# Performance work log

Hardware: AMD Instinct MI355X
Metric: run time of the kernel (lower is better)

Reference implementation:

```python
import jax, jax.numpy as jnp
import numpy as np

D_MODEL = 1024
N_HEAD = 16
HEAD_DIM = D_MODEL // N_HEAD  # 64


def setup_inputs() -> dict:
    key = jax.random.key(0)
    ks = jax.random.split(key, 8)
    B, T, C = 4, 2048, D_MODEL
    s = 0.02
    return {
        "q": jax.random.normal(ks[0], (B, T, C), jnp.float32),
        "k": jax.random.normal(ks[1], (B, T, C), jnp.float32),
        "v": jax.random.normal(ks[2], (B, T, C), jnp.float32),
        "Wq": jax.random.normal(ks[3], (C, C), jnp.float32) * s,
        "Wk": jax.random.normal(ks[4], (C, HEAD_DIM), jnp.float32) * s,
        "Wv": jax.random.normal(ks[5], (C, HEAD_DIM), jnp.float32) * s,
        "Wp": jax.random.normal(ks[6], (C, C), jnp.float32) * s,
        "bp": jnp.zeros((C,), jnp.float32),
    }


def reference(q, k, v, Wq, Wk, Wv, Wp, bp):
    B, T, C = q.shape
    scale = 1.0 / jnp.sqrt(jnp.asarray(HEAD_DIM, q.dtype))
    # projections (torch Linear: x @ W.T, here weights stored as [in, out])
    q_proj = (q @ Wq).reshape(B, T, N_HEAD, HEAD_DIM)  # [B,T,H,D]
    k_proj = k @ Wk  # [B,T,D] single shared KV head
    v_proj = v @ Wv  # [B,T,D]
    # full O(T^2) scores per head, shared K
    wei = jnp.einsum("bqhd,bkd->bhqk", q_proj, k_proj) * scale  # [B,H,T,T]
    p = jax.nn.softmax(wei, axis=-1)
    out = jnp.einsum("bhqk,bkd->bqhd", p, v_proj).reshape(B, T, C)
    return out @ Wp + bp  # dropout p=0.0 -> identity
```

## Files before the change

kernel.cpp:

```cpp
#include <hip/hip_runtime.h>
#include <hip/hip_bf16.h>


#define B_ 4
#define T_ 2048
#define C_ 1024
#define H_ 16
#define D_ 64
#define BT_ (B_*T_)
#define CS_ 0.1803368801111204f

typedef short bfrag __attribute__((ext_vector_type(8)));
typedef float f32x4 __attribute__((ext_vector_type(4)));
typedef __bf16 bf2_t __attribute__((ext_vector_type(2)));

static __device__ inline short f2bf(float f){
    union { __bf16 h; short s; } c; c.h = (__bf16)f;
    return c.s;
}
static __device__ inline unsigned pk2(float a, float b){
    union { bf2_t v; unsigned u; } c;
    c.v[0] = (__bf16)a; c.v[1] = (__bf16)b;
    return c.u;
}

#if __has_builtin(__builtin_amdgcn_global_load_lds)
#define GLL16(g,l) __builtin_amdgcn_global_load_lds(                              \
    (const __attribute__((address_space(1))) void*)(g),                           \
    (__attribute__((address_space(3))) void*)(l), 16, 0, 0)
#else
#define GLL16(g,l) (*(uint4*)(l) = *(const uint4*)(g))
#endif

#if __has_builtin(__builtin_amdgcn_exp2f)
#define EXP2(x) __builtin_amdgcn_exp2f(x)
#else
#define EXP2(x) __expf((x)*0.693147180559945f)
#endif

__global__ __launch_bounds__(256) void prep_kernel(
    const float* __restrict__ Wq, const float* __restrict__ Wk,
    const float* __restrict__ Wv, const float* __restrict__ Wp,
    short* __restrict__ WqT, short* __restrict__ WkT,
    short* __restrict__ WvT, short* __restrict__ WpT)
{
    int b2 = blockIdx.x, tid = threadIdx.x;
    __shared__ short Ls[64][65];
    const float* W; short* Wt; int N, idx;
    if (b2 < 256)      { W = Wq; Wt = WqT; N = 1024; idx = b2; }
    else if (b2 < 272) { W = Wk; Wt = WkT; N = 64;   idx = b2 - 256; }
    else if (b2 < 288) { W = Wv; Wt = WvT; N = 64;   idx = b2 - 272; }
    else               { W = Wp; Wt = WpT; N = 1024; idx = b2 - 288; }
    int nx = N >> 6;
    int n0 = (idx % nx) * 64, k0 = (idx / nx) * 64;
    {
        int kr = tid >> 2, c4 = (tid & 3) * 16;
        const float* g = W + (size_t)(k0 + kr) * N + n0 + c4;
        #pragma unroll
        for (int e = 0; e < 16; e++) Ls[kr][c4 + e] = f2bf(g[e]);
    }
    __syncthreads();
    {
        int nr = tid >> 2, kc = (tid & 3) * 16;
        __align__(16) short tmp[16];
        #pragma unroll
        for (int e = 0; e < 16; e++) tmp[e] = Ls[kc + e][nr];
        short* o = Wt + (size_t)(n0 + nr) * 1024 + k0 + kc;
        *(uint4*)(o)     = *(uint4*)tmp;
        *(uint4*)(o + 8) = *(uint4*)(tmp + 8);
    }
}

__global__ __launch_bounds__(256) void proj_kernel(
    const float* __restrict__ Aq, const float* __restrict__ Ksrc,
    const float* __restrict__ Vsrc,
    const short* __restrict__ WqT, const short* __restrict__ WkT,
    const short* __restrict__ WvT,
    short* __restrict__ Qp, short* __restrict__ Kfo, short* __restrict__ Vfo)
{
    __shared__ __align__(16) short lds[16384];
    int bx = blockIdx.x, tid = threadIdx.x;
    int w = tid >> 6, lane = tid & 63;
    int quad = lane >> 4, l16 = lane & 15;

    if (bx < 512) {
        short* As = lds;
        short* Bs = lds + 8192;
        const int K = C_;
        int wm = (w >> 1) * 64, wn = (w & 1) * 64;
        int m0 = (bx & 63) * 128, n0 = (bx >> 6) * 128;

        const float* gA[8]; short* lA[8];
        #pragma unroll
        for (int i = 0; i < 8; i++) {
            int c = tid + 256 * i;
            int row = c >> 4, fc = c & 15;
            gA[i] = Aq + (size_t)(m0 + row) * K + fc * 4;
            int m16 = row >> 4, l16r = row & 15;
            int ks = fc >> 3, q4 = (fc >> 1) & 3, e0 = (fc & 1) * 4;
            lA[i] = As + ((m16 * 2 + ks) * 64 + l16r * 4 + q4) * 8 + e0;
        }
        const short* gB[4]; short* lB[4];
        #pragma unroll
        for (int i = 0; i < 4; i++) {
            int c = tid + 256 * i;
            int row = ((c >> 7) << 4) + ((c & 63) >> 2);
            int koff = ((c >> 6) & 1) * 32 + (c & 3) * 8;
            gB[i] = WqT + (size_t)(n0 + row) * K + koff;
            lB[i] = Bs + c * 8;
        }

        f32x4 acc[4][4] = {};
        for (int k0 = 0; k0 < K; k0 += 64) {
            __syncthreads();
            #pragma unroll
            for (int i = 0; i < 8; i++) {
                float4 f = *(const float4*)(gA[i] + k0);
                uint2 p; p.x = pk2(f.x, f.y); p.y = pk2(f.z, f.w);
                *(uint2*)lA[i] = p;
            }
            #pragma unroll
            for (int i = 0; i < 4; i++) GLL16(gB[i] + k0, lB[i]);
            __syncthreads();
            #pragma unroll
            for (int ks = 0; ks < 2; ks++) {
                bfrag af[4], bf[4];
                #pragma unroll
                for (int i = 0; i < 4; i++)
                    af[i] = *(const bfrag*)(As + ((((wm >> 4) + i) * 2 + ks) * 64 + l16 * 4 + quad) * 8);
                #pragma unroll
                for (int i = 0; i < 4; i++)
                    bf[i] = *(const bfrag*)(Bs + ((((wn >> 4) + i) * 2 + ks) * 64 + l16 * 4 + quad) * 8);
                #pragma unroll
                for (int mi = 0; mi < 4; mi++)
                    #pragma unroll
                    for (int ni = 0; ni < 4; ni++)
                        acc[mi][ni] = __builtin_amdgcn_mfma_f32_16x16x32_bf16(af[mi], bf[ni], acc[mi][ni], 0, 0, 0);
            }
        }
        #pragma unroll
        for (int mi = 0; mi < 4; mi++)
            #pragma unroll
            for (int ni = 0; ni < 4; ni++) {
                int col = n0 + wn + ni * 16 + l16;
                #pragma unroll
                for (int r = 0; r < 4; r++) {
                    int row = m0 + wm + mi * 16 + quad * 4 + r;
                    Qp[(size_t)row * C_ + col] = f2bf(acc[mi][ni][r] * CS_);
                }
            }
        return;
    }

    {
        short* As = lds;
        short* Bs = lds + 2048;
        int idx2 = bx - 512;
        int mode = idx2 >> 8;
        int m0 = (idx2 & 255) * 32;
        const float* A  = mode ? Vsrc : Ksrc;
        const short* Bt = mode ? WvT : WkT;
        short* Out      = mode ? Vfo : Kfo;

        int wrow = (w >> 1) * 16, wcol = (w & 1) * 32;

        int arow = tid >> 3, acol = (tid & 7) * 8;
        int akh = acol >> 5, aoct = (acol >> 3) & 3;
        short* asl = As + ((((arow >> 4) * 2 + akh) * 64 + (arow & 15) * 4 + aoct) * 8);
        const float* ag = A + (size_t)(m0 + arow) * C_ + acol;
        int brow = tid >> 2, bcol = (tid & 3) * 16;
        int bkh = bcol >> 5, boct = (bcol >> 3) & 3;
        short* bsl = Bs + ((((brow >> 4) * 2 + bkh) * 64 + (brow & 15) * 4 + boct) * 8);
        const short* bg = Bt + (size_t)brow * C_ + bcol;

        f32x4 acc[2] = {};
        for (int k0 = 0; k0 < C_; k0 += 64) {
            __syncthreads();
            {
                float4 fa = *(const float4*)(ag + k0);
                float4 fb = *(const float4*)(ag + k0 + 4);
                uint4 pa; pa.x = pk2(fa.x,fa.y); pa.y = pk2(fa.z,fa.w);
                          pa.z = pk2(fb.x,fb.y); pa.w = pk2(fb.z,fb.w);
                *(uint4*)asl = pa;
                uint4 t0 = *(const uint4*)(bg + k0);
                uint4 t1 = *(const uint4*)(bg + k0 + 8);
                *(uint4*)bsl = t0; *(uint4*)(bsl + 8) = t1;
            }
            __syncthreads();
            #pragma unroll
            for (int ks = 0; ks < 2; ks++) {
                bfrag af = *(const bfrag*)(As + (((wrow >> 4) * 2 + ks) * 64 + l16 * 4 + quad) * 8);
                #pragma unroll
                for (int ni = 0; ni < 2; ni++) {
                    int n = wcol + ni * 16;
                    bfrag bf = *(const bfrag*)(Bs + (((n >> 4) * 2 + ks) * 64 + l16 * 4 + quad) * 8);
                    acc[ni] = __builtin_amdgcn_mfma_f32_16x16x32_bf16(af, bf, acc[ni], 0, 0, 0);
                }
            }
        }
        if (mode == 0) {
            #pragma unroll
            for (int ni = 0; ni < 2; ni++)
                #pragma unroll
                for (int r = 0; r < 4; r++) {
                    int key = m0 + wrow + quad * 4 + r;
                    int d = wcol + ni * 16 + l16;
                    size_t adr = (size_t)(key >> 6) * 4096 +
                        ((((d >> 5) * 4 + ((key >> 4) & 3)) * 4 + ((d >> 3) & 3)) * 16 + (key & 15)) * 8 + (d & 7);
                    Out[adr] = f2bf(acc[ni][r]);
                }
        } else {
            #pragma unroll
            for (int ni = 0; ni < 2; ni++) {
                int ni2 = (w & 1) * 2 + ni;
                int key = m0 + wrow + quad * 4;
                int tile = key >> 6, kfk = (key >> 5) & 1, qv = (key >> 3) & 3;
                int jb = (quad & 1) * 4;
                uint2 pk; pk.x = pk2(acc[ni][0], acc[ni][1]); pk.y = pk2(acc[ni][2], acc[ni][3]);
                *(uint2*)(Out + (size_t)tile * 4096 + (((kfk * 4 + ni2) * 4 + qv) * 16 + l16) * 8 + jb) = pk;
            }
        }
    }
}

__global__ __launch_bounds__(1024, 4) void attn_kernel(
    const short* __restrict__ Qp, const short* __restrict__ Kfo,
    const short* __restrict__ Vfo, short* __restrict__ Out)
{
    __shared__ __align__(16) short lds[49152];
    int qb = blockIdx.x, hg = blockIdx.y, b = blockIdx.z;
    int tid = threadIdx.x, w = tid >> 6, lane = tid & 63;
    int quad = lane >> 4, l16 = lane & 15;
    int h = hg * 4 + (w >> 2);
    int wq = (w & 3) * 32;
    short* Ps = lds + 16384 + w * 2048;
    int m0q = b * T_ + qb * 128;

    bfrag qf[2][2];
    #pragma unroll
    for (int nb = 0; nb < 2; nb++)
        #pragma unroll
        for (int kf = 0; kf < 2; kf++)
            qf[nb][kf] = *(const bfrag*)(Qp +
                (size_t)(m0q + wq + nb * 16 + l16) * C_ + h * 64 + kf * 32 + quad * 8);

    const short* Kb = Kfo + (size_t)b * (T_ * D_);
    const short* Vb = Vfo + (size_t)b * (T_ * D_);
    int q0 = qb * 128 + wq;

    f32x4 o[4][2] = {};
    float lsum[2] = {0.f, 0.f};
    int fragoff = (quad * 16 + l16) * 8;
    int st8 = tid * 8;

    {
        const short* s0 = (tid < 512) ? Kb : (Vb - 4096);
        GLL16(s0 + st8, lds + st8);
    }
    __syncthreads();

    for (int t = 0; t < T_ / 64; t++) {
        short* bc = lds + (t & 1) * 8192;
        if (t + 1 < T_ / 64) {
            short* bn = lds + ((t + 1) & 1) * 8192;
            const short* Kt = Kb + (t + 1) * 4096;
            const short* Vt = Vb + (t + 1) * 4096;
            const short* sn = (tid < 512) ? Kt : (Vt - 4096);
            GLL16(sn + st8, bn + st8);
        }
        bfrag ka[2][4];
        #pragma unroll
        for (int kf = 0; kf < 2; kf++)
            #pragma unroll
            for (int mi = 0; mi < 4; mi++)
                ka[kf][mi] = *(const bfrag*)(bc + (kf * 4 + mi) * 512 + fragoff);
        f32x4 s[4][2];
        #pragma unroll
        for (int mi = 0; mi < 4; mi++)
            #pragma unroll
            for (int nb = 0; nb < 2; nb++) {
                f32x4 z = {};
                z = __builtin_amdgcn_mfma_f32_16x16x32_bf16(ka[0][mi], qf[nb][0], z, 0, 0, 0);
                s[mi][nb] = __builtin_amdgcn_mfma_f32_16x16x32_bf16(ka[1][mi], qf[nb][1], z, 0, 0, 0);
            }
        bfrag va[2][4];
        #pragma unroll
        for (int kf = 0; kf < 2; kf++)
            #pragma unroll
            for (int mi = 0; mi < 4; mi++)
                va[kf][mi] = *(const bfrag*)(bc + 4096 + (kf * 4 + mi) * 512 + fragoff);
        #pragma unroll
        for (int nb = 0; nb < 2; nb++) {
            #pragma unroll
            for (int mi = 0; mi < 4; mi++) {
                float p0 = EXP2(s[mi][nb][0]);
                float p1 = EXP2(s[mi][nb][1]);
                float p2 = EXP2(s[mi][nb][2]);
                float p3 = EXP2(s[mi][nb][3]);
                lsum[nb] += (p0 + p1) + (p2 + p3);
                uint2 pk; pk.x = pk2(p0, p1); pk.y = pk2(p2, p3);
                int kf = mi >> 1, qp_ = (mi & 1) * 2 + (quad >> 1), jb = (quad & 1) * 4;
                *(uint2*)(Ps + (kf * 2 + nb) * 512 + qp_ * 128 + l16 * 8 + jb) = pk;
            }
        }
        #pragma unroll
        for (int nb = 0; nb < 2; nb++) {
            bfrag pf0 = *(const bfrag*)(Ps + (0 + nb) * 512 + quad * 128 + l16 * 8);
            bfrag pf1 = *(const bfrag*)(Ps + (2 + nb) * 512 + quad * 128 + l16 * 8);
            #pragma unroll
            for (int mi = 0; mi < 4; mi++) {
                o[mi][nb] = __builtin_amdgcn_mfma_f32_16x16x32_bf16(va[0][mi], pf0, o[mi][nb], 0, 0, 0);
                o[mi][nb] = __builtin_amdgcn_mfma_f32_16x16x32_bf16(va[1][mi], pf1, o[mi][nb], 0, 0, 0);
            }
        }
        __syncthreads();
    }
    #pragma unroll
    for (int nb = 0; nb < 2; nb++) {
        float l = lsum[nb];
        l += __shfl_xor(l, 16, 64);
        l += __shfl_xor(l, 32, 64);
        float rl = 1.0f / l;
        size_t row = (size_t)(b * T_ + q0 + nb * 16 + l16);
        #pragma unroll
        for (int mi = 0; mi < 4; mi++) {
            uint2 pk; pk.x = pk2(o[mi][nb][0] * rl, o[mi][nb][1] * rl);
                      pk.y = pk2(o[mi][nb][2] * rl, o[mi][nb][3] * rl);
            *(uint2*)(Out + row * C_ + h * 64 + mi * 16 + quad * 4) = pk;
        }
    }
}

__global__ __launch_bounds__(256) void gemm_fin_kernel(
    const short* __restrict__ A, const short* __restrict__ Bt,
    const float* __restrict__ bias, float* __restrict__ Out)
{
    __shared__ __align__(16) short As[8192];
    __shared__ __align__(16) short Bs[8192];
    const int N = C_, K = C_;
    int tid = threadIdx.x, w = tid >> 6, lane = tid & 63;
    int quad = lane >> 4, l16 = lane & 15;
    int wm = (w >> 1) * 64, wn = (w & 1) * 64;
    int m0 = blockIdx.x * 128, n0 = blockIdx.y * 128;

    const short* gA[4]; short* lA[4];
    const short* gB[4]; short* lB[4];
    #pragma unroll
    for (int i = 0; i < 4; i++) {
        int c = tid + 256 * i;
        int row = ((c >> 7) << 4) + ((c & 63) >> 2);
        int koff = ((c >> 6) & 1) * 32 + (c & 3) * 8;
        gA[i] = A + (size_t)(m0 + row) * K + koff;
        lA[i] = As + c * 8;
        gB[i] = Bt + (size_t)(n0 + row) * K + koff;
        lB[i] = Bs + c * 8;
    }

    f32x4 acc[4][4] = {};
    for (int k0 = 0; k0 < K; k0 += 64) {
        __syncthreads();
        #pragma unroll
        for (int i = 0; i < 4; i++) GLL16(gA[i] + k0, lA[i]);
        #pragma unroll
        for (int i = 0; i < 4; i++) GLL16(gB[i] + k0, lB[i]);
        __syncthreads();
        #pragma unroll
        for (int ks = 0; ks < 2; ks++) {
            bfrag af[4], bf[4];
            #pragma unroll
            for (int i = 0; i < 4; i++)
                af[i] = *(const bfrag*)(As + ((((wm >> 4) + i) * 2 + ks) * 64 + l16 * 4 + quad) * 8);
            #pragma unroll
            for (int i = 0; i < 4; i++)
                bf[i] = *(const bfrag*)(Bs + ((((wn >> 4) + i) * 2 + ks) * 64 + l16 * 4 + quad) * 8);
            #pragma unroll
            for (int mi = 0; mi < 4; mi++)
                #pragma unroll
                for (int ni = 0; ni < 4; ni++)
                    acc[mi][ni] = __builtin_amdgcn_mfma_f32_16x16x32_bf16(af[mi], bf[ni], acc[mi][ni], 0, 0, 0);
        }
    }
    #pragma unroll
    for (int mi = 0; mi < 4; mi++)
        #pragma unroll
        for (int ni = 0; ni < 4; ni++) {
            int col = n0 + wn + ni * 16 + l16;
            float bv = bias[col];
            #pragma unroll
            for (int r = 0; r < 4; r++) {
                int row = m0 + wm + mi * 16 + quad * 4 + r;
                Out[(size_t)row * N + col] = acc[mi][ni][r] + bv;
            }
        }
}

extern "C" void kernel_launch(void* const* d_in, const int* in_sizes, int n_in,
                              void* d_out, int out_size, void* d_ws, size_t ws_size,
                              hipStream_t stream) {
    const float* q  = (const float*)d_in[0];
    const float* k  = (const float*)d_in[1];
    const float* v  = (const float*)d_in[2];
    const float* Wq = (const float*)d_in[3];
    const float* Wk = (const float*)d_in[4];
    const float* Wv = (const float*)d_in[5];
    const float* Wp = (const float*)d_in[6];
    const float* bp = (const float*)d_in[7];
    float* out = (float*)d_out;

    char* ws = (char*)d_ws;
    short* Qp       = (short*)(ws);
    short* attn_out = (short*)(ws + (16u << 20));
    short* WqT  = (short*)(ws + (32u << 20));
    short* WpT  = (short*)(ws + (34u << 20));
    short* Kfo  = (short*)(ws + (36u << 20));
    short* Vfo  = (short*)(ws + (37u << 20));
    short* WkT  = (short*)(ws + (38u << 20));
    short* WvT  = (short*)(ws + (38u << 20) + (1u << 18));

    dim3 blk(256);
    prep_kernel<<<544, blk, 0, stream>>>(Wq, Wk, Wv, Wp, WqT, WkT, WvT, WpT);
    proj_kernel<<<1024, blk, 0, stream>>>(q, k, v, WqT, WkT, WvT, Qp, Kfo, Vfo);
    attn_kernel<<<dim3(16, 4, 4), dim3(1024), 0, stream>>>(Qp, Kfo, Vfo, attn_out);
    gemm_fin_kernel<<<dim3(64, 8), blk, 0, stream>>>(attn_out, WpT, bp, out);
}
```

Before: 277.5 us.

## Prefetch projection loads into registers, halve attention block size, MFMA row sums

```diff
diff --git a/kernel.cpp b/kernel.cpp
--- a/kernel.cpp
+++ b/kernel.cpp
@@ -110,17 +110,24 @@
             lB[i] = Bs + c * 8;
         }
 
+        float4 fA[8];
+        #pragma unroll
+        for (int i = 0; i < 8; i++) fA[i] = *(const float4*)(gA[i]);
+
         f32x4 acc[4][4] = {};
         for (int k0 = 0; k0 < K; k0 += 64) {
             __syncthreads();
             #pragma unroll
             for (int i = 0; i < 8; i++) {
-                float4 f = *(const float4*)(gA[i] + k0);
-                uint2 p; p.x = pk2(f.x, f.y); p.y = pk2(f.z, f.w);
+                uint2 p; p.x = pk2(fA[i].x, fA[i].y); p.y = pk2(fA[i].z, fA[i].w);
                 *(uint2*)lA[i] = p;
             }
             #pragma unroll
             for (int i = 0; i < 4; i++) GLL16(gB[i] + k0, lB[i]);
+            if (k0 + 64 < K) {
+                #pragma unroll
+                for (int i = 0; i < 8; i++) fA[i] = *(const float4*)(gA[i] + k0 + 64);
+            }
             __syncthreads();
             #pragma unroll
             for (int ks = 0; ks < 2; ks++) {
@@ -173,18 +180,25 @@
         short* bsl = Bs + ((((brow >> 4) * 2 + bkh) * 64 + (brow & 15) * 4 + boct) * 8);
         const short* bg = Bt + (size_t)brow * C_ + bcol;
 
+        float4 fa = *(const float4*)(ag);
+        float4 fb = *(const float4*)(ag + 4);
+        uint4 t0 = *(const uint4*)(bg);
+        uint4 t1 = *(const uint4*)(bg + 8);
+
         f32x4 acc[2] = {};
         for (int k0 = 0; k0 < C_; k0 += 64) {
             __syncthreads();
             {
-                float4 fa = *(const float4*)(ag + k0);
-                float4 fb = *(const float4*)(ag + k0 + 4);
                 uint4 pa; pa.x = pk2(fa.x,fa.y); pa.y = pk2(fa.z,fa.w);
                           pa.z = pk2(fb.x,fb.y); pa.w = pk2(fb.z,fb.w);
                 *(uint4*)asl = pa;
-                uint4 t0 = *(const uint4*)(bg + k0);
-                uint4 t1 = *(const uint4*)(bg + k0 + 8);
                 *(uint4*)bsl = t0; *(uint4*)(bsl + 8) = t1;
+            }
+            if (k0 + 64 < C_) {
+                fa = *(const float4*)(ag + k0 + 64);
+                fb = *(const float4*)(ag + k0 + 68);
+                t0 = *(const uint4*)(bg + k0 + 64);
+                t1 = *(const uint4*)(bg + k0 + 72);
             }
             __syncthreads();
             #pragma unroll
@@ -223,15 +237,15 @@
     }
 }
 
-__global__ __launch_bounds__(1024, 4) void attn_kernel(
+__global__ __launch_bounds__(512, 4) void attn_kernel(
     const short* __restrict__ Qp, const short* __restrict__ Kfo,
     const short* __restrict__ Vfo, short* __restrict__ Out)
 {
-    __shared__ __align__(16) short lds[49152];
+    __shared__ __align__(16) short lds[32768];
     int qb = blockIdx.x, hg = blockIdx.y, b = blockIdx.z;
     int tid = threadIdx.x, w = tid >> 6, lane = tid & 63;
     int quad = lane >> 4, l16 = lane & 15;
-    int h = hg * 4 + (w >> 2);
+    int h = hg * 2 + (w >> 2);
     int wq = (w & 3) * 32;
     short* Ps = lds + 16384 + w * 2048;
     int m0q = b * T_ + qb * 128;
@@ -249,24 +263,24 @@
     int q0 = qb * 128 + wq;
 
     f32x4 o[4][2] = {};
-    float lsum[2] = {0.f, 0.f};
+    f32x4 lacc[2] = {};
+    bfrag ones;
+    #pragma unroll
+    for (int e = 0; e < 8; e++) ones[e] = (short)0x3F80;
+
     int fragoff = (quad * 16 + l16) * 8;
     int st8 = tid * 8;
 
-    {
-        const short* s0 = (tid < 512) ? Kb : (Vb - 4096);
-        GLL16(s0 + st8, lds + st8);
-    }
+    GLL16(Kb + st8, lds + st8);
+    GLL16(Vb + st8, lds + 4096 + st8);
     __syncthreads();
 
     for (int t = 0; t < T_ / 64; t++) {
         short* bc = lds + (t & 1) * 8192;
         if (t + 1 < T_ / 64) {
             short* bn = lds + ((t + 1) & 1) * 8192;
-            const short* Kt = Kb + (t + 1) * 4096;
-            const short* Vt = Vb + (t + 1) * 4096;
-            const short* sn = (tid < 512) ? Kt : (Vt - 4096);
-            GLL16(sn + st8, bn + st8);
+            GLL16(Kb + (t + 1) * 4096 + st8, bn + st8);
+            GLL16(Vb + (t + 1) * 4096 + st8, bn + 4096 + st8);
         }
         bfrag ka[2][4];
         #pragma unroll
@@ -297,7 +311,6 @@
                 float p1 = EXP2(s[mi][nb][1]);
                 float p2 = EXP2(s[mi][nb][2]);
                 float p3 = EXP2(s[mi][nb][3]);
-                lsum[nb] += (p0 + p1) + (p2 + p3);
                 uint2 pk; pk.x = pk2(p0, p1); pk.y = pk2(p2, p3);
                 int kf = mi >> 1, qp_ = (mi & 1) * 2 + (quad >> 1), jb = (quad & 1) * 4;
                 *(uint2*)(Ps + (kf * 2 + nb) * 512 + qp_ * 128 + l16 * 8 + jb) = pk;
@@ -312,15 +325,14 @@
                 o[mi][nb] = __builtin_amdgcn_mfma_f32_16x16x32_bf16(va[0][mi], pf0, o[mi][nb], 0, 0, 0);
                 o[mi][nb] = __builtin_amdgcn_mfma_f32_16x16x32_bf16(va[1][mi], pf1, o[mi][nb], 0, 0, 0);
             }
+            lacc[nb] = __builtin_amdgcn_mfma_f32_16x16x32_bf16(ones, pf0, lacc[nb], 0, 0, 0);
+            lacc[nb] = __builtin_amdgcn_mfma_f32_16x16x32_bf16(ones, pf1, lacc[nb], 0, 0, 0);
         }
         __syncthreads();
     }
     #pragma unroll
     for (int nb = 0; nb < 2; nb++) {
-        float l = lsum[nb];
-        l += __shfl_xor(l, 16, 64);
-        l += __shfl_xor(l, 32, 64);
-        float rl = 1.0f / l;
+        float rl = 1.0f / lacc[nb][0];
         size_t row = (size_t)(b * T_ + q0 + nb * 16 + l16);
         #pragma unroll
         for (int mi = 0; mi < 4; mi++) {
@@ -420,6 +432,6 @@
     dim3 blk(256);
     prep_kernel<<<544, blk, 0, stream>>>(Wq, Wk, Wv, Wp, WqT, WkT, WvT, WpT);
     proj_kernel<<<1024, blk, 0, stream>>>(q, k, v, WqT, WkT, WvT, Qp, Kfo, Vfo);
-    attn_kernel<<<dim3(16, 4, 4), dim3(1024), 0, stream>>>(Qp, Kfo, Vfo, attn_out);
+    attn_kernel<<<dim3(16, 8, 4), dim3(512), 0, stream>>>(Qp, Kfo, Vfo, attn_out);
     gemm_fin_kernel<<<dim3(64, 8), blk, 0, stream>>>(attn_out, WpT, bp, out);
 }
```

Result: faster. 266.2 us (-4.1%).
